# Performance work log

Hardware: AMD Instinct MI355X
Metric: run time of the kernel (lower is better)

The kernel has to match this reference:

```python
import jax, jax.numpy as jnp
import numpy as np

B, CIN, H, W = 4, 64, 160, 160
G, K = 8, 3
KK = K * K
PAD = K // 2
CG = CIN // G  # channels per deformable group


def setup_inputs() -> dict:
    key = jax.random.key(0)
    ks = jax.random.split(key, 6)
    x = jax.random.normal(ks[0], (B, CIN, H, W), jnp.float32)
    feat = jax.random.normal(ks[1], (B, CIN, H, W), jnp.float32)
    # conv_offset weights (zero-init in the original; small random here so offsets are nontrivial)
    w_off = jax.random.normal(ks[2], (3 * G * KK, CIN, 3, 3), jnp.float32) * 0.01
    b_off = jax.random.normal(ks[3], (3 * G * KK,), jnp.float32) * 0.01
    # deformable conv weights (torchvision DeformConv2d: groups=1, bias=True)
    w_dcn = jax.random.normal(ks[4], (CIN, CIN, K, K), jnp.float32) * (1.0 / np.sqrt(CIN * KK))
    b_dcn = jax.random.normal(ks[5], (CIN,), jnp.float32) * 0.01
    return dict(x=x, feat=feat, w_off=w_off, b_off=b_off, w_dcn=w_dcn, b_dcn=b_dcn)


def _modulated_deform_conv(x, offset, mask, w, b):
    # x: [B,C,H,W]; offset: [B,2*G*KK,H,W] (interleaved dy,dx per (g,k));
    # mask: [B,G*KK,H,W]; w: [Cout,C,K,K]; stride 1, zero padding K//2.
    Bn, C, Hh, Ww = x.shape
    off = offset.reshape(Bn, G, KK, 2, Hh, Ww)
    dy = off[:, :, :, 0]  # [B,G,KK,H,W]
    dx = off[:, :, :, 1]
    ki = jnp.arange(K)
    base_y = (jnp.repeat(ki, K) - PAD).reshape(1, 1, KK, 1, 1).astype(x.dtype)
    base_x = (jnp.tile(ki, K) - PAD).reshape(1, 1, KK, 1, 1).astype(x.dtype)
    hy = jnp.arange(Hh, dtype=x.dtype).reshape(1, 1, 1, Hh, 1)
    wx = jnp.arange(Ww, dtype=x.dtype).reshape(1, 1, 1, 1, Ww)
    py = hy + base_y + dy  # sample rows  [B,G,KK,H,W]
    px = wx + base_x + dx  # sample cols
    y0 = jnp.floor(py)
    x0 = jnp.floor(px)
    ly = py - y0
    lx = px - x0
    y0i = y0.astype(jnp.int32)
    x0i = x0.astype(jnp.int32)
    xg = x.reshape(Bn, G, CG, Hh * Ww)

    def gather(yi, xi):
        valid = ((yi >= 0) & (yi < Hh) & (xi >= 0) & (xi < Ww)).astype(x.dtype)
        idx = jnp.clip(yi, 0, Hh - 1) * Ww + jnp.clip(xi, 0, Ww - 1)
        flat = idx.reshape(Bn, G, 1, KK * Hh * Ww)
        v = jnp.take_along_axis(xg, flat, axis=3).reshape(Bn, G, CG, KK, Hh, Ww)
        return v * valid[:, :, None]  # zero padding outside

    v = ((1 - ly) * (1 - lx))[:, :, None] * gather(y0i, x0i) \
      + ((1 - ly) * lx)[:, :, None] * gather(y0i, x0i + 1) \
      + (ly * (1 - lx))[:, :, None] * gather(y0i + 1, x0i) \
      + (ly * lx)[:, :, None] * gather(y0i + 1, x0i + 1)
    v = v * mask.reshape(Bn, G, 1, KK, Hh, Ww)
    wr = w.reshape(w.shape[0], G, CG, KK)
    out = jnp.einsum('ogck,bgckhw->bohw', wr, v) + b[None, :, None, None]
    return out


def reference(x, feat, w_off, b_off, w_dcn, b_dcn):
    # conv_offset: 3x3 conv, stride 1, pad 1
    out = jax.lax.conv_general_dilated(
        feat, w_off, (1, 1), ((1, 1), (1, 1)),
        dimension_numbers=('NCHW', 'OIHW', 'NCHW')) + b_off[None, :, None, None]
    o1, o2, m = jnp.split(out, 3, axis=1)
    offset = jnp.concatenate([o1, o2], axis=1)  # [B, 2*G*KK, H, W]
    mask = jax.nn.sigmoid(m)                    # [B, G*KK, H, W]
    return _modulated_deform_conv(x, offset, mask, w_dcn, b_dcn)
```

## Files before the change

### kernel.cpp

```cpp
#include <hip/hip_runtime.h>
#include <math.h>

#define Bn   4
#define CINc 64
#define Hh   160
#define Ww   160
#define Gg   8
#define HW   (Hh * Ww)
#define COFF 216

#define OROW 220
#define VROW 200
#define OFFS_SZ (64 * OROW)
#define UNION_SZ 12800

typedef short bf16x8 __attribute__((ext_vector_type(8)));
typedef float f32x4  __attribute__((ext_vector_type(4)));

static __device__ __forceinline__ unsigned short f2bf(float f) {
    unsigned int u = __float_as_uint(f);
    u = (u + 0x7fffu + ((u >> 16) & 1u)) >> 16;
    return (unsigned short)u;
}
static __device__ __forceinline__ float bf2f(unsigned short s) {
    return __uint_as_float(((unsigned int)s) << 16);
}
static __device__ __forceinline__ float blo(unsigned int u) {
    return __uint_as_float(u << 16);
}
static __device__ __forceinline__ float bhi(unsigned int u) {
    return __uint_as_float(u & 0xffff0000u);
}

#define WB 180
__global__ __launch_bounds__(256)
void prep_kernel(const float* __restrict__ feat, const float* __restrict__ x,
                 const float* __restrict__ w_off, const float* __restrict__ w_dcn,
                 unsigned short* __restrict__ featT, unsigned short* __restrict__ xG,
                 unsigned short* __restrict__ wofrag, unsigned short* __restrict__ wfrag) {
    const int blk = blockIdx.x;
    const int t = threadIdx.x;
    if (blk < 1280) {
        __shared__ float tile[CINc][161];
        const int isx = blk >= 640;
        const int rem = isx ? blk - 640 : blk;
        const int b = rem / Hh;
        const int h = rem % Hh;
        const float* src = isx ? x : feat;
        for (int i = t; i < CINc * Ww; i += 256) {
            int ci = i / Ww, w = i % Ww;
            tile[ci][w] = src[(((size_t)b * CINc + ci) * Hh + h) * Ww + w];
        }
        __syncthreads();
        if (isx) {
            for (int i = t; i < CINc * Ww; i += 256) {
                int g = i / (Ww * 8);
                int r = i % (Ww * 8);
                int w = r >> 3, cg = r & 7;
                xG[(((size_t)b * Gg + g) * HW + h * Ww + w) * 8 + cg] = f2bf(tile[g * 8 + cg][w]);
            }
        } else {
            for (int i = t; i < CINc * Ww; i += 256) {
                int w = i / CINc, ci = i % CINc;
                featT[(((size_t)b * Hh + h) * Ww + w) * CINc + ci] = f2bf(tile[ci][w]);
            }
        }
    } else {
        for (int e = (blk - 1280) * 256 + t; e < 147456 + 36864; e += WB * 256) {
            if (e < 147456) {
                const int j    = e & 7;
                const int lane = (e >> 3) & 63;
                const int rest = e >> 9;
                const int mt = rest & 15;
                const int q  = rest >> 4;
                const int ks = q & 1;
                const int kp = q >> 1;
                const int co = mt * 16 + (lane & 15);
                const int ci = ks * 32 + (lane >> 4) * 8 + j;
                float v = (co < COFF) ? w_off[(size_t)co * 576 + ci * 9 + kp] : 0.f;
                wofrag[e] = f2bf(v);
            } else {
                const int e2   = e - 147456;
                const int j    = e2 & 7;
                const int lane = (e2 >> 3) & 63;
                const int mt   = (e2 >> 9) & 3;
                const int ks   = e2 >> 11;
                const int m = mt * 16 + (lane & 15);
                const int k = ks * 32 + (lane >> 4) * 8 + j;
                const int g = k / 72, r = k % 72;
                const int kk = r >> 3, cg = r & 7;
                const int ci = g * 8 + cg;
                wfrag[e2] = f2bf(w_dcn[((size_t)m * CINc + ci) * 9 + kk]);
            }
        }
    }
}

__global__ __launch_bounds__(256, 3)
void dcnpack_fused(const unsigned short* __restrict__ featT,
                   const unsigned short* __restrict__ xG,
                   const unsigned short* __restrict__ wofrag,
                   const unsigned short* __restrict__ wfrag,
                   const float* __restrict__ b_off,
                   const float* __restrict__ b_dcn,
                   float* __restrict__ out) {
    __shared__ unsigned short smem[OFFS_SZ + UNION_SZ];
    unsigned short* offs = smem;
    unsigned short* halo = smem + OFFS_SZ;
    unsigned short* vbuf = smem + OFFS_SZ;

    const int b  = blockIdx.z;
    const int h0 = blockIdx.y * 8;
    const int w0 = blockIdx.x * 8;
    const int t  = threadIdx.x;
    const int wv   = t >> 6;
    const int lane = t & 63;
    const int n    = lane & 15;
    const int kg   = lane >> 4;

    for (int task = t; task < 800; task += 256) {
        const int pix = task >> 3, ch = task & 7;
        const int ry = pix / 10, rx = pix % 10;
        const int gh = h0 - 1 + ry, gw = w0 - 1 + rx;
        float4 v = make_float4(0.f, 0.f, 0.f, 0.f);
        if (gh >= 0 && gh < Hh && gw >= 0 && gw < Ww)
            v = *(const float4*)(featT + ((((size_t)b * Hh) + gh) * Ww + gw) * CINc + ch * 8);
        *(float4*)(halo + pix * 72 + ch * 8) = v;
    }
    __syncthreads();

    const int bbase0 = (((n >> 3) * 10) + (n & 7)) * 72 + kg * 8;

    f32x4 cacc[4][4] = {};
    #pragma unroll
    for (int s = 0; s < 18; ++s) {
        const int kp = s >> 1, ks = s & 1;
        const int ky = kp / 3, kx = kp % 3;
        bf16x8 af[4];
        #pragma unroll
        for (int i = 0; i < 4; ++i)
            af[i] = *(const bf16x8*)(wofrag +
                (((size_t)(kp * 2 + ks) * 16 + wv + 4 * i) * 64 + lane) * 8);
        #pragma unroll
        for (int nt = 0; nt < 4; ++nt) {
            const bf16x8 bfr = *(const bf16x8*)(halo + bbase0 + nt * 1440 +
                                                (ky * 10 + kx) * 72 + ks * 32);
            #pragma unroll
            for (int i = 0; i < 4; ++i)
                cacc[i][nt] = __builtin_amdgcn_mfma_f32_16x16x32_bf16(af[i], bfr, cacc[i][nt], 0, 0, 0);
        }
    }

    #pragma unroll
    for (int i = 0; i < 4; ++i) {
        const int mt = wv + 4 * i;
        #pragma unroll
        for (int r = 0; r < 4; ++r) {
            const int co = mt * 16 + kg * 4 + r;
            if (co < COFF) {
                const float bias = b_off[co];
                const int ismask = (co >= 144);
                const int gk = ismask ? (co - 144) : (co >> 1);
                const int type = ismask ? 2 : (co & 1);
                #pragma unroll
                for (int nt = 0; nt < 4; ++nt) {
                    const int p = nt * 16 + n;
                    float v = cacc[i][nt][r] + bias;
                    if (ismask) v = 1.f / (1.f + expf(-v));
                    offs[p * OROW + gk * 3 + type] = f2bf(v);
                }
            }
        }
    }
    __syncthreads();

    f32x4 dacc[4] = {};

    for (int c = 0; c < 3; ++c) {
        #pragma unroll 3
        for (int it = 0; it < 6; ++it) {
            const int task = t + it * 256;
            const int p    = task & 63;
            const int u    = c * 24 + (task >> 6);
            const int g    = u / 9;
            const int k    = u % 9;
            const int h = h0 + (p >> 3);
            const int w = w0 + (p & 7);

            const float dy   = bf2f(offs[p * OROW + u * 3 + 0]);
            const float dx   = bf2f(offs[p * OROW + u * 3 + 1]);
            const float mask = bf2f(offs[p * OROW + u * 3 + 2]);

            const float py  = (float)h + (float)(k / 3 - 1) + dy;
            const float pxx = (float)w + (float)(k % 3 - 1) + dx;
            const float y0f = floorf(py), x0f = floorf(pxx);
            const float ly = py - y0f, lx = pxx - x0f;
            const int y0 = (int)y0f, x0i = (int)x0f;
            const int y1 = y0 + 1,  x1  = x0i + 1;

            const float vy0 = (y0 >= 0 && y0 < Hh) ? 1.f : 0.f;
            const float vy1 = (y1 >= 0 && y1 < Hh) ? 1.f : 0.f;
            const float vx0 = (x0i >= 0 && x0i < Ww) ? 1.f : 0.f;
            const float vx1 = (x1 >= 0 && x1 < Ww) ? 1.f : 0.f;

            const float c00 = (1.f - ly) * (1.f - lx) * vy0 * vx0 * mask;
            const float c01 = (1.f - ly) * lx         * vy0 * vx1 * mask;
            const float c10 = ly         * (1.f - lx) * vy1 * vx0 * mask;
            const float c11 = ly         * lx         * vy1 * vx1 * mask;

            const int y0c = min(max(y0, 0), Hh - 1), y1c = min(max(y1, 0), Hh - 1);
            const int x0c = min(max(x0i, 0), Ww - 1), x1c = min(max(x1, 0), Ww - 1);

            const unsigned short* xb = xG + ((size_t)b * Gg + g) * HW * 8;
            const uint4 q00 = *(const uint4*)(xb + ((size_t)y0c * Ww + x0c) * 8);
            const uint4 q01 = *(const uint4*)(xb + ((size_t)y0c * Ww + x1c) * 8);
            const uint4 q10 = *(const uint4*)(xb + ((size_t)y1c * Ww + x0c) * 8);
            const uint4 q11 = *(const uint4*)(xb + ((size_t)y1c * Ww + x1c) * 8);
            const unsigned int a00[4] = {q00.x, q00.y, q00.z, q00.w};
            const unsigned int a01[4] = {q01.x, q01.y, q01.z, q01.w};
            const unsigned int a10[4] = {q10.x, q10.y, q10.z, q10.w};
            const unsigned int a11[4] = {q11.x, q11.y, q11.z, q11.w};

            unsigned short res[8];
            #pragma unroll
            for (int j = 0; j < 4; ++j) {
                const float vl = c00 * blo(a00[j]) + c01 * blo(a01[j])
                               + c10 * blo(a10[j]) + c11 * blo(a11[j]);
                const float vh = c00 * bhi(a00[j]) + c01 * bhi(a01[j])
                               + c10 * bhi(a10[j]) + c11 * bhi(a11[j]);
                res[2 * j]     = f2bf(vl);
                res[2 * j + 1] = f2bf(vh);
            }
            *(uint4*)(vbuf + (size_t)p * VROW + (u - c * 24) * 8) = *(const uint4*)res;
        }
        __syncthreads();

        #pragma unroll
        for (int s = 0; s < 6; ++s) {
            const int ksg = c * 6 + s;
            const bf16x8 afr = *(const bf16x8*)(wfrag + (((size_t)ksg * 4 + wv) * 64 + lane) * 8);
            #pragma unroll
            for (int nt = 0; nt < 4; ++nt) {
                const bf16x8 bfr = *(const bf16x8*)(vbuf + (nt * 16 + n) * VROW + s * 32 + kg * 8);
                dacc[nt] = __builtin_amdgcn_mfma_f32_16x16x32_bf16(afr, bfr, dacc[nt], 0, 0, 0);
            }
        }
        __syncthreads();
    }

    #pragma unroll
    for (int nt = 0; nt < 4; ++nt) {
        const int p = nt * 16 + n;
        const int h = h0 + (p >> 3);
        const int w = w0 + (p & 7);
        #pragma unroll
        for (int r = 0; r < 4; ++r) {
            const int o = wv * 16 + kg * 4 + r;
            out[(((size_t)b * CINc + o) * HW) + h * Ww + w] = dacc[nt][r] + b_dcn[o];
        }
    }
}

extern "C" void kernel_launch(void* const* d_in, const int* in_sizes, int n_in,
                              void* d_out, int out_size, void* d_ws, size_t ws_size,
                              hipStream_t stream) {
    const float* x     = (const float*)d_in[0];
    const float* feat  = (const float*)d_in[1];
    const float* w_off = (const float*)d_in[2];
    const float* b_off = (const float*)d_in[3];
    const float* w_dcn = (const float*)d_in[4];
    const float* b_dcn = (const float*)d_in[5];
    float* out = (float*)d_out;

    unsigned short* featT  = (unsigned short*)d_ws;
    unsigned short* xG     = featT + (size_t)Bn * HW * CINc;
    unsigned short* wofrag = xG + (size_t)Bn * HW * CINc;
    unsigned short* wfrag  = wofrag + (size_t)147456;

    prep_kernel<<<dim3(1280 + WB), 256, 0, stream>>>(
        feat, x, w_off, w_dcn, featT, xG, wofrag, wfrag);
    dcnpack_fused<<<dim3(Ww / 8, Hh / 8, Bn), 256, 0, stream>>>(
        featT, xG, wofrag, wfrag, b_off, b_dcn, out);
}
```

Before: 214.2 us.

## Build deform-conv B fragments in registers and software-pipeline the bilinear gathers

Removes the shared-memory vbuf staging of sampled values. Each lane now computes the bilinear-sampled bf16 fragment for its own pixel and K-slice directly in registers and feeds it to MFMA. The next step's gathers are prefetched while the current step computes. Offsets are stored with a stride of 4 so they load as one ushort4, the halo and offsets buffers now share one smaller smem region (allowing 4 blocks per CU), and the per-chunk barriers are dropped. The trade-off is higher register pressure from the prefetch, plus truncation instead of round-to-nearest when packing to bf16.

```diff
diff --git a/kernel.cpp b/kernel.cpp
--- a/kernel.cpp
+++ b/kernel.cpp
@@ -9,10 +9,8 @@
 #define HW   (Hh * Ww)
 #define COFF 216
 
-#define OROW 220
-#define VROW 200
-#define OFFS_SZ (64 * OROW)
-#define UNION_SZ 12800
+#define OROW 292
+#define SMEM_USH (64 * OROW)
 
 typedef short bf16x8 __attribute__((ext_vector_type(8)));
 typedef float f32x4  __attribute__((ext_vector_type(4)));
@@ -96,7 +94,7 @@
     }
 }
 
-__global__ __launch_bounds__(256, 3)
+__global__ __launch_bounds__(256, 4)
 void dcnpack_fused(const unsigned short* __restrict__ featT,
                    const unsigned short* __restrict__ xG,
                    const unsigned short* __restrict__ wofrag,
@@ -104,10 +102,9 @@
                    const float* __restrict__ b_off,
                    const float* __restrict__ b_dcn,
                    float* __restrict__ out) {
-    __shared__ unsigned short smem[OFFS_SZ + UNION_SZ];
+    __shared__ unsigned short smem[SMEM_USH];
+    unsigned short* halo = smem;
     unsigned short* offs = smem;
-    unsigned short* halo = smem + OFFS_SZ;
-    unsigned short* vbuf = smem + OFFS_SZ;
 
     const int b  = blockIdx.z;
     const int h0 = blockIdx.y * 8;
@@ -130,7 +127,6 @@
     __syncthreads();
 
     const int bbase0 = (((n >> 3) * 10) + (n & 7)) * 72 + kg * 8;
-
     f32x4 cacc[4][4] = {};
     #pragma unroll
     for (int s = 0; s < 18; ++s) {
@@ -150,6 +146,7 @@
                 cacc[i][nt] = __builtin_amdgcn_mfma_f32_16x16x32_bf16(af[i], bfr, cacc[i][nt], 0, 0, 0);
         }
     }
+    __syncthreads();
 
     #pragma unroll
     for (int i = 0; i < 4; ++i) {
@@ -167,96 +164,94 @@
                     const int p = nt * 16 + n;
                     float v = cacc[i][nt][r] + bias;
                     if (ismask) v = 1.f / (1.f + expf(-v));
-                    offs[p * OROW + gk * 3 + type] = f2bf(v);
+                    offs[p * OROW + gk * 4 + type] = f2bf(v);
                 }
             }
         }
     }
     __syncthreads();
 
+    const int pfix = wv * 16 + n;
+    const int hh = h0 + (pfix >> 3);
+    const int ww = w0 + (pfix & 7);
+    const unsigned short* offrow = offs + pfix * OROW;
+    const unsigned short* xbb = xG + (size_t)b * Gg * HW * 8;
+
     f32x4 dacc[4] = {};
-
-    for (int c = 0; c < 3; ++c) {
-        #pragma unroll 3
-        for (int it = 0; it < 6; ++it) {
-            const int task = t + it * 256;
-            const int p    = task & 63;
-            const int u    = c * 24 + (task >> 6);
-            const int g    = u / 9;
-            const int k    = u % 9;
-            const int h = h0 + (p >> 3);
-            const int w = w0 + (p & 7);
-
-            const float dy   = bf2f(offs[p * OROW + u * 3 + 0]);
-            const float dx   = bf2f(offs[p * OROW + u * 3 + 1]);
-            const float mask = bf2f(offs[p * OROW + u * 3 + 2]);
-
-            const float py  = (float)h + (float)(k / 3 - 1) + dy;
-            const float pxx = (float)w + (float)(k % 3 - 1) + dx;
-            const float y0f = floorf(py), x0f = floorf(pxx);
-            const float ly = py - y0f, lx = pxx - x0f;
-            const int y0 = (int)y0f, x0i = (int)x0f;
-            const int y1 = y0 + 1,  x1  = x0i + 1;
-
-            const float vy0 = (y0 >= 0 && y0 < Hh) ? 1.f : 0.f;
-            const float vy1 = (y1 >= 0 && y1 < Hh) ? 1.f : 0.f;
-            const float vx0 = (x0i >= 0 && x0i < Ww) ? 1.f : 0.f;
-            const float vx1 = (x1 >= 0 && x1 < Ww) ? 1.f : 0.f;
-
-            const float c00 = (1.f - ly) * (1.f - lx) * vy0 * vx0 * mask;
-            const float c01 = (1.f - ly) * lx         * vy0 * vx1 * mask;
-            const float c10 = ly         * (1.f - lx) * vy1 * vx0 * mask;
-            const float c11 = ly         * lx         * vy1 * vx1 * mask;
-
-            const int y0c = min(max(y0, 0), Hh - 1), y1c = min(max(y1, 0), Hh - 1);
-            const int x0c = min(max(x0i, 0), Ww - 1), x1c = min(max(x1, 0), Ww - 1);
-
-            const unsigned short* xb = xG + ((size_t)b * Gg + g) * HW * 8;
-            const uint4 q00 = *(const uint4*)(xb + ((size_t)y0c * Ww + x0c) * 8);
-            const uint4 q01 = *(const uint4*)(xb + ((size_t)y0c * Ww + x1c) * 8);
-            const uint4 q10 = *(const uint4*)(xb + ((size_t)y1c * Ww + x0c) * 8);
-            const uint4 q11 = *(const uint4*)(xb + ((size_t)y1c * Ww + x1c) * 8);
-            const unsigned int a00[4] = {q00.x, q00.y, q00.z, q00.w};
-            const unsigned int a01[4] = {q01.x, q01.y, q01.z, q01.w};
-            const unsigned int a10[4] = {q10.x, q10.y, q10.z, q10.w};
-            const unsigned int a11[4] = {q11.x, q11.y, q11.z, q11.w};
-
-            unsigned short res[8];
+    uint4 gq[4];
+    float cf[4];
+
+    auto prep = [&](int ksit, uint4* gqo, float* cfo) {
+        const int u = ksit * 4 + kg;
+        const int g = (u * 57) >> 9;
+        const int k = u - 9 * g;
+        const int ky = (k * 11) >> 5;
+        const int kx = k - 3 * ky;
+        const ushort4 o4 = *(const ushort4*)(offrow + u * 4);
+        const float dy = bf2f(o4.x), dx = bf2f(o4.y), m = bf2f(o4.z);
+        const float py  = (float)(hh + ky - 1) + dy;
+        const float pxx = (float)(ww + kx - 1) + dx;
+        const float y0f = floorf(py), x0f = floorf(pxx);
+        const float ly = py - y0f, lx = pxx - x0f;
+        const int y0 = (int)y0f, x0i = (int)x0f;
+        const int y1 = y0 + 1, x1 = x0i + 1;
+        const float vy0 = (y0 >= 0 && y0 < Hh) ? 1.f : 0.f;
+        const float vy1 = (y1 >= 0 && y1 < Hh) ? 1.f : 0.f;
+        const float vx0 = (x0i >= 0 && x0i < Ww) ? 1.f : 0.f;
+        const float vx1 = (x1 >= 0 && x1 < Ww) ? 1.f : 0.f;
+        cfo[0] = (1.f - ly) * (1.f - lx) * vy0 * vx0 * m;
+        cfo[1] = (1.f - ly) * lx         * vy0 * vx1 * m;
+        cfo[2] = ly         * (1.f - lx) * vy1 * vx0 * m;
+        cfo[3] = ly         * lx         * vy1 * vx1 * m;
+        const int y0c = min(max(y0, 0), Hh - 1), y1c = min(max(y1, 0), Hh - 1);
+        const int x0c = min(max(x0i, 0), Ww - 1), x1c = min(max(x1, 0), Ww - 1);
+        const unsigned short* xb = xbb + (size_t)g * HW * 8;
+        gqo[0] = *(const uint4*)(xb + ((size_t)(y0c * Ww + x0c)) * 8);
+        gqo[1] = *(const uint4*)(xb + ((size_t)(y0c * Ww + x1c)) * 8);
+        gqo[2] = *(const uint4*)(xb + ((size_t)(y1c * Ww + x0c)) * 8);
+        gqo[3] = *(const uint4*)(xb + ((size_t)(y1c * Ww + x1c)) * 8);
+    };
+
+    prep(0, gq, cf);
+    #pragma unroll 2
+    for (int ks = 0; ks < 18; ++ks) {
+        bf16x8 af[4];
+        #pragma unroll
+        for (int mt = 0; mt < 4; ++mt)
+            af[mt] = *(const bf16x8*)(wfrag + (((size_t)ks * 4 + mt) * 64 + lane) * 8);
+
+        uint4 gqn[4]; float cfn[4];
+        if (ks < 17) prep(ks + 1, gqn, cfn);
+
+        const unsigned int a0[4] = {gq[0].x, gq[0].y, gq[0].z, gq[0].w};
+        const unsigned int a1[4] = {gq[1].x, gq[1].y, gq[1].z, gq[1].w};
+        const unsigned int a2[4] = {gq[2].x, gq[2].y, gq[2].z, gq[2].w};
+        const unsigned int a3[4] = {gq[3].x, gq[3].y, gq[3].z, gq[3].w};
+        union { unsigned int u[4]; bf16x8 v; } pk;
+        #pragma unroll
+        for (int j = 0; j < 4; ++j) {
+            const float vl = cf[0] * blo(a0[j]) + cf[1] * blo(a1[j])
+                           + cf[2] * blo(a2[j]) + cf[3] * blo(a3[j]);
+            const float vh = cf[0] * bhi(a0[j]) + cf[1] * bhi(a1[j])
+                           + cf[2] * bhi(a2[j]) + cf[3] * bhi(a3[j]);
+            pk.u[j] = __builtin_amdgcn_perm(__float_as_uint(vh), __float_as_uint(vl), 0x07060302u);
+        }
+        #pragma unroll
+        for (int mt = 0; mt < 4; ++mt)
+            dacc[mt] = __builtin_amdgcn_mfma_f32_16x16x32_bf16(af[mt], pk.v, dacc[mt], 0, 0, 0);
+
+        if (ks < 17) {
             #pragma unroll
-            for (int j = 0; j < 4; ++j) {
-                const float vl = c00 * blo(a00[j]) + c01 * blo(a01[j])
-                               + c10 * blo(a10[j]) + c11 * blo(a11[j]);
-                const float vh = c00 * bhi(a00[j]) + c01 * bhi(a01[j])
-                               + c10 * bhi(a10[j]) + c11 * bhi(a11[j]);
-                res[2 * j]     = f2bf(vl);
-                res[2 * j + 1] = f2bf(vh);
-            }
-            *(uint4*)(vbuf + (size_t)p * VROW + (u - c * 24) * 8) = *(const uint4*)res;
-        }
-        __syncthreads();
-
-        #pragma unroll
-        for (int s = 0; s < 6; ++s) {
-            const int ksg = c * 6 + s;
-            const bf16x8 afr = *(const bf16x8*)(wfrag + (((size_t)ksg * 4 + wv) * 64 + lane) * 8);
-            #pragma unroll
-            for (int nt = 0; nt < 4; ++nt) {
-                const bf16x8 bfr = *(const bf16x8*)(vbuf + (nt * 16 + n) * VROW + s * 32 + kg * 8);
-                dacc[nt] = __builtin_amdgcn_mfma_f32_16x16x32_bf16(afr, bfr, dacc[nt], 0, 0, 0);
-            }
-        }
-        __syncthreads();
+            for (int i2 = 0; i2 < 4; ++i2) { gq[i2] = gqn[i2]; cf[i2] = cfn[i2]; }
+        }
     }
 
     #pragma unroll
-    for (int nt = 0; nt < 4; ++nt) {
-        const int p = nt * 16 + n;
-        const int h = h0 + (p >> 3);
-        const int w = w0 + (p & 7);
+    for (int mt = 0; mt < 4; ++mt) {
         #pragma unroll
         for (int r = 0; r < 4; ++r) {
-            const int o = wv * 16 + kg * 4 + r;
-            out[(((size_t)b * CINc + o) * HW) + h * Ww + w] = dacc[nt][r] + b_dcn[o];
+            const int o = mt * 16 + kg * 4 + r;
+            out[((size_t)b * CINc + o) * HW + hh * Ww + ww] = dacc[mt][r] + b_dcn[o];
         }
     }
 }
```

Result: no change. 218.1 us (+1.8%).
